# Kernel tuning notes

Hardware: AMD Instinct MI355X
Metric: run time of the kernel (lower is better)

## Reference

```python
import jax, jax.numpy as jnp
import numpy as np

SIREN_OMEGA_0 = 30.0
EPS = 1e-4


def setup_inputs() -> dict:
    key = jax.random.key(0)
    ks = jax.random.split(key, 10)
    B, N, M, IN, OUT = 2, 16384, 1024, 256, 256
    x = jax.random.normal(ks[0], (B, N, IN), dtype=jnp.float32)
    query_coords = jax.random.normal(ks[1], (B, N, 3), dtype=jnp.float32)
    atomic_coords = jax.random.normal(ks[2], (B, M, 3), dtype=jnp.float32)
    # SIREN init (not is_first): bound = sqrt(6/in)/omega_0
    bound = (6.0 / IN) ** 0.5 / SIREN_OMEGA_0
    W = jax.random.uniform(ks[3], (OUT, IN), jnp.float32, -bound, bound)
    b = jax.random.uniform(ks[4], (OUT,), jnp.float32, -bound, bound)
    # freq_net: Linear(3,16) -> Softplus -> Linear(16,1), default torch init
    b1l = 1.0 / np.sqrt(3.0)
    fw1 = jax.random.uniform(ks[5], (16, 3), jnp.float32, -b1l, b1l)
    fb1 = jax.random.uniform(ks[6], (16,), jnp.float32, -b1l, b1l)
    b2l = 1.0 / np.sqrt(16.0)
    fw2 = jax.random.uniform(ks[7], (1, 16), jnp.float32, -b2l, b2l)
    fb2 = jax.random.uniform(ks[8], (1,), jnp.float32, -b2l, b2l)
    return {"x": x, "query_coords": query_coords, "atomic_coords": atomic_coords,
            "W": W, "b": b, "fw1": fw1, "fb1": fb1, "fw2": fw2, "fb2": fb2}


def reference(x, query_coords, atomic_coords, W, b, fw1, fb1, fw2, fb2):
    omega_base = SIREN_OMEGA_0
    # pre_activation = x @ W^T + b : [B, N, OUT]
    pre = jnp.einsum('bni,oi->bno', x, W) + b
    # freq_net(query_coords): Linear -> softplus -> Linear, clamp [0,5], nan->0
    h = jax.nn.softplus(jnp.einsum('bnd,hd->bnh', query_coords, fw1) + fb1)
    local_scale = jnp.einsum('bnh,oh->bno', h, fw2) + fb2  # [B, N, 1]
    local_scale = jnp.nan_to_num(jnp.clip(local_scale, 0.0, 5.0), nan=0.0)
    # pairwise distance [B, N, M] via broadcasted diff, then min over atoms
    diff = query_coords[:, :, None, :] - atomic_coords[:, None, :, :]  # [B,N,M,3]
    dist = jnp.sqrt(jnp.maximum(jnp.sum(diff * diff, axis=-1), EPS))
    min_dist = jnp.min(dist, axis=-1, keepdims=True)  # [B, N, 1]
    omega = omega_base * (1.0 + local_scale * jnp.exp(-min_dist))
    return jnp.sin(omega * pre)
```

## Files before the change

### kernel.cpp

```cpp
#include <hip/hip_runtime.h>
#include <hip/hip_bf16.h>

#define NPTS    32768
#define K_DIM   256
#define O_DIM   256
#define M_ATOMS 1024

typedef __attribute__((ext_vector_type(8))) short short8;
typedef __attribute__((ext_vector_type(4))) float f32x4;

__device__ __forceinline__ unsigned short bf16_rn(float f) {
  unsigned u = __float_as_uint(f);
  unsigned r = u + 0x7FFFu + ((u >> 16) & 1u);
  return (unsigned short)(r >> 16);
}

__device__ __forceinline__ void cvt8(const f32x4 f0, const f32x4 f1,
                                     short8* h, short8* l) {
#pragma unroll
  for (int j = 0; j < 4; ++j) {
    unsigned short h0 = bf16_rn(f0[j]);
    (*h)[j] = (short)h0;
    (*l)[j] = (short)bf16_rn(f0[j] - __uint_as_float((unsigned)h0 << 16));
    unsigned short h1 = bf16_rn(f1[j]);
    (*h)[j + 4] = (short)h1;
    (*l)[j + 4] = (short)bf16_rn(f1[j] - __uint_as_float((unsigned)h1 << 16));
  }
}

__device__ __forceinline__ void async16(void* l, const void* g) {
  __builtin_amdgcn_global_load_lds(
      (const __attribute__((address_space(1))) void*)g,
      (__attribute__((address_space(3))) void*)l, 16, 0, 0);
}

__global__ __launch_bounds__(256) void wprep_kernel(const float* __restrict__ W,
                                                    unsigned short* __restrict__ whF,
                                                    unsigned short* __restrict__ wlF) {
  int t = blockIdx.x * 256 + threadIdx.x;
  int lane = t & 63;
  int ct = (t >> 6) & 15;
  int kc = t >> 10;
  int col = ct * 16 + (lane & 15);
  int k0 = kc * 32 + (lane >> 4) * 8;
  const float* src = W + (size_t)col * K_DIM + k0;
  f32x4 f0 = *(const f32x4*)(src);
  f32x4 f1 = *(const f32x4*)(src + 4);
  short8 h, l;
  cvt8(f0, f1, &h, &l);
  *(short8*)(whF + (size_t)t * 8) = h;
  *(short8*)(wlF + (size_t)t * 8) = l;
}

__global__ __launch_bounds__(256, 2) void fused_kernel(
    const float* __restrict__ x, const float* __restrict__ qc,
    const float* __restrict__ atoms,
    const unsigned short* __restrict__ whF, const unsigned short* __restrict__ wlF,
    const float* __restrict__ bias,
    const float* __restrict__ fw1, const float* __restrict__ fb1,
    const float* __restrict__ fw2, const float* __restrict__ fb2,
    float* __restrict__ out) {
  __shared__ f32x4 bsh[2][2048];
  char* ldsC = (char*)&bsh[0][0];
  const int lane = threadIdx.x & 63;
  const int wave = threadIdx.x >> 6;
  const int lrow = lane & 15;
  const int lk = lane >> 4;
  const int pbase = blockIdx.x * 64 + wave * 16;
  const int row = pbase + lrow;

  float bias_r[16];
#pragma unroll
  for (int ct = 0; ct < 16; ++ct) bias_r[ct] = bias[ct * 16 + lrow];

  const char* whB = (const char*)whF;
  const char* wlB = (const char*)wlF;
  const int toff = wave * 1024 + lane * 16;

  {
    char* db = ldsC;
    const char* gh = whB + toff;
    const char* gl = wlB + toff;
#pragma unroll
    for (int j = 0; j < 4; ++j) {
      async16(db + j * 4096 + wave * 1024, gh + j * 4096);
      async16(db + 16384 + j * 4096 + wave * 1024, gl + j * 4096);
    }
  }

  const float* xr = x + (size_t)row * K_DIM + lk * 8;
  f32x4 a0 = *(const f32x4*)(xr);
  f32x4 a1 = *(const f32x4*)(xr + 4);
  short8 ahi, alo;
  cvt8(a0, a1, &ahi, &alo);

  f32x4 acc[16];
#pragma unroll
  for (int ct = 0; ct < 16; ++ct) acc[ct] = (f32x4){0.f, 0.f, 0.f, 0.f};

  __syncthreads();

  int cur = 0;
  f32x4 a0n, a1n;
#pragma unroll 1
  for (int it = 0; it < 8; ++it) {
    if (it < 7) {
      char* db = ldsC + (cur ^ 1) * 32768;
      const char* gh = whB + (it + 1) * 16384 + toff;
      const char* gl = wlB + (it + 1) * 16384 + toff;
#pragma unroll
      for (int j = 0; j < 4; ++j) {
        async16(db + j * 4096 + wave * 1024, gh + j * 4096);
        async16(db + 16384 + j * 4096 + wave * 1024, gl + j * 4096);
      }
      const float* xn = x + (size_t)row * K_DIM + (it + 1) * 32 + lk * 8;
      a0n = *(const f32x4*)(xn);
      a1n = *(const f32x4*)(xn + 4);
    }
    const char* bp = ldsC + cur * 32768;
#pragma unroll
    for (int ct = 0; ct < 16; ++ct) {
      short8 bh = *(const short8*)(bp + ct * 1024 + lane * 16);
      short8 bl = *(const short8*)(bp + 16384 + ct * 1024 + lane * 16);
      acc[ct] = __builtin_amdgcn_mfma_f32_16x16x32_bf16(ahi, bh, acc[ct], 0, 0, 0);
      acc[ct] = __builtin_amdgcn_mfma_f32_16x16x32_bf16(alo, bh, acc[ct], 0, 0, 0);
      acc[ct] = __builtin_amdgcn_mfma_f32_16x16x32_bf16(ahi, bl, acc[ct], 0, 0, 0);
    }
    __syncthreads();
    if (it < 7) {
      cvt8(a0n, a1n, &ahi, &alo);
      cur ^= 1;
    }
  }

  const int batch = pbase >> 14;
  const float* A = atoms + (size_t)batch * M_ATOMS * 3;
  f32x4* at4 = (f32x4*)ldsC;
  for (int i = threadIdx.x; i < M_ATOMS; i += 256) {
    const float* ap = A + i * 3;
    float ax = ap[0], ay = ap[1], az = ap[2];
    f32x4 v = {ax, ay, az, ax * ax + ay * ay + az * az};
    at4[i] = v;
  }
  __syncthreads();

  const int pt = pbase + lrow;
  const float qx = qc[(size_t)pt * 3 + 0];
  const float qy = qc[(size_t)pt * 3 + 1];
  const float qz = qc[(size_t)pt * 3 + 2];
  float m0 = 3.0e38f, m1 = 3.0e38f, m2 = 3.0e38f, m3 = 3.0e38f;
  const int i0 = lk * 256;
  for (int i = i0; i < i0 + 256; i += 4) {
    f32x4 v0 = at4[i + 0], v1 = at4[i + 1], v2 = at4[i + 2], v3 = at4[i + 3];
    float d;
    d = v0[0] * qx; d = __fmaf_rn(v0[1], qy, d); d = __fmaf_rn(v0[2], qz, d);
    m0 = fminf(m0, __fmaf_rn(d, -2.0f, v0[3]));
    d = v1[0] * qx; d = __fmaf_rn(v1[1], qy, d); d = __fmaf_rn(v1[2], qz, d);
    m1 = fminf(m1, __fmaf_rn(d, -2.0f, v1[3]));
    d = v2[0] * qx; d = __fmaf_rn(v2[1], qy, d); d = __fmaf_rn(v2[2], qz, d);
    m2 = fminf(m2, __fmaf_rn(d, -2.0f, v2[3]));
    d = v3[0] * qx; d = __fmaf_rn(v3[1], qy, d); d = __fmaf_rn(v3[2], qz, d);
    m3 = fminf(m3, __fmaf_rn(d, -2.0f, v3[3]));
  }
  float md = fminf(fminf(m0, m1), fminf(m2, m3));
  md = fminf(md, __shfl_xor(md, 16));
  md = fminf(md, __shfl_xor(md, 32));
  md += qx * qx + qy * qy + qz * qz;
  float mind = sqrtf(fmaxf(md, 1.0e-4f));

  float facc = fb2[0];
#pragma unroll
  for (int j = 0; j < 16; ++j) {
    float z = fw1[j * 3 + 0] * qx + fw1[j * 3 + 1] * qy + fw1[j * 3 + 2] * qz + fb1[j];
    facc += fw2[j] * log1pf(__expf(z));
  }
  float ls = fminf(fmaxf(facc, 0.0f), 5.0f);
  float omega_l = 30.0f * (1.0f + ls * __expf(-mind));

  float om[4];
#pragma unroll
  for (int j = 0; j < 4; ++j) om[j] = __shfl(omega_l, lk * 4 + j);

#pragma unroll
  for (int ct = 0; ct < 16; ++ct) {
#pragma unroll
    for (int j = 0; j < 4; ++j) {
      float pre = acc[ct][j] + bias_r[ct];
      out[(size_t)(pbase + lk * 4 + j) * O_DIM + ct * 16 + lrow] = __sinf(om[j] * pre);
    }
  }
}

extern "C" void kernel_launch(void* const* d_in, const int* in_sizes, int n_in,
                              void* d_out, int out_size, void* d_ws, size_t ws_size,
                              hipStream_t stream) {
  (void)in_sizes; (void)n_in; (void)out_size; (void)ws_size;
  const float* x     = (const float*)d_in[0];
  const float* qc    = (const float*)d_in[1];
  const float* atoms = (const float*)d_in[2];
  const float* W     = (const float*)d_in[3];
  const float* b     = (const float*)d_in[4];
  const float* fw1   = (const float*)d_in[5];
  const float* fb1   = (const float*)d_in[6];
  const float* fw2   = (const float*)d_in[7];
  const float* fb2   = (const float*)d_in[8];
  float* out = (float*)d_out;

  unsigned short* whF = (unsigned short*)d_ws;
  unsigned short* wlF = whF + 65536;

  wprep_kernel<<<32, 256, 0, stream>>>(W, whF, wlF);
  fused_kernel<<<512, 256, 0, stream>>>(x, qc, atoms, whF, wlF, b,
                                        fw1, fb1, fw2, fb2, out);
}
```

Before: 119.5 us.

## Split waves into 2x2 point/column tiles to halve B-fragment LDS reads

Each wave now computes 32 points by 128 output columns instead of 16 points by 256 columns. Every B fragment read from LDS is reused across two A row-tiles, which halves LDS read traffic per MFMA. The x loads per wave double and the min-distance search is split across the wave pair, whose partial minima are now combined through LDS with an extra barrier. The MFMA count and accumulator register count stay the same.

```diff
diff --git a/kernel.cpp b/kernel.cpp
--- a/kernel.cpp
+++ b/kernel.cpp
@@ -64,14 +64,15 @@
   char* ldsC = (char*)&bsh[0][0];
   const int lane = threadIdx.x & 63;
   const int wave = threadIdx.x >> 6;
+  const int ptile = wave >> 1;
+  const int ch = wave & 1;
   const int lrow = lane & 15;
   const int lk = lane >> 4;
-  const int pbase = blockIdx.x * 64 + wave * 16;
-  const int row = pbase + lrow;
-
-  float bias_r[16];
-#pragma unroll
-  for (int ct = 0; ct < 16; ++ct) bias_r[ct] = bias[ct * 16 + lrow];
+  const int pbase = blockIdx.x * 64 + ptile * 32;
+
+  float bias_r[8];
+#pragma unroll
+  for (int ct = 0; ct < 8; ++ct) bias_r[ct] = bias[(ch * 8 + ct) * 16 + lrow];
 
   const char* whB = (const char*)whF;
   const char* wlB = (const char*)wlF;
@@ -88,20 +89,22 @@
     }
   }
 
-  const float* xr = x + (size_t)row * K_DIM + lk * 8;
-  f32x4 a0 = *(const f32x4*)(xr);
-  f32x4 a1 = *(const f32x4*)(xr + 4);
-  short8 ahi, alo;
-  cvt8(a0, a1, &ahi, &alo);
+  const float* xr0 = x + (size_t)(pbase + lrow) * K_DIM + lk * 8;
+  const float* xr1 = x + (size_t)(pbase + 16 + lrow) * K_DIM + lk * 8;
+  f32x4 a00 = *(const f32x4*)(xr0), a01 = *(const f32x4*)(xr0 + 4);
+  f32x4 a10 = *(const f32x4*)(xr1), a11 = *(const f32x4*)(xr1 + 4);
+  short8 ahi0, alo0, ahi1, alo1;
+  cvt8(a00, a01, &ahi0, &alo0);
+  cvt8(a10, a11, &ahi1, &alo1);
 
   f32x4 acc[16];
 #pragma unroll
-  for (int ct = 0; ct < 16; ++ct) acc[ct] = (f32x4){0.f, 0.f, 0.f, 0.f};
+  for (int i = 0; i < 16; ++i) acc[i] = (f32x4){0.f, 0.f, 0.f, 0.f};
 
   __syncthreads();
 
   int cur = 0;
-  f32x4 a0n, a1n;
+  f32x4 n00, n01, n10, n11;
 #pragma unroll 1
   for (int it = 0; it < 8; ++it) {
     if (it < 7) {
@@ -113,22 +116,27 @@
         async16(db + j * 4096 + wave * 1024, gh + j * 4096);
         async16(db + 16384 + j * 4096 + wave * 1024, gl + j * 4096);
       }
-      const float* xn = x + (size_t)row * K_DIM + (it + 1) * 32 + lk * 8;
-      a0n = *(const f32x4*)(xn);
-      a1n = *(const f32x4*)(xn + 4);
-    }
-    const char* bp = ldsC + cur * 32768;
-#pragma unroll
-    for (int ct = 0; ct < 16; ++ct) {
+      const float* p0 = xr0 + (it + 1) * 32;
+      const float* p1 = xr1 + (it + 1) * 32;
+      n00 = *(const f32x4*)(p0); n01 = *(const f32x4*)(p0 + 4);
+      n10 = *(const f32x4*)(p1); n11 = *(const f32x4*)(p1 + 4);
+    }
+    const char* bp = ldsC + cur * 32768 + ch * 8192;
+#pragma unroll
+    for (int ct = 0; ct < 8; ++ct) {
       short8 bh = *(const short8*)(bp + ct * 1024 + lane * 16);
       short8 bl = *(const short8*)(bp + 16384 + ct * 1024 + lane * 16);
-      acc[ct] = __builtin_amdgcn_mfma_f32_16x16x32_bf16(ahi, bh, acc[ct], 0, 0, 0);
-      acc[ct] = __builtin_amdgcn_mfma_f32_16x16x32_bf16(alo, bh, acc[ct], 0, 0, 0);
-      acc[ct] = __builtin_amdgcn_mfma_f32_16x16x32_bf16(ahi, bl, acc[ct], 0, 0, 0);
+      acc[ct]     = __builtin_amdgcn_mfma_f32_16x16x32_bf16(ahi0, bh, acc[ct],     0, 0, 0);
+      acc[8 + ct] = __builtin_amdgcn_mfma_f32_16x16x32_bf16(ahi1, bh, acc[8 + ct], 0, 0, 0);
+      acc[ct]     = __builtin_amdgcn_mfma_f32_16x16x32_bf16(alo0, bh, acc[ct],     0, 0, 0);
+      acc[8 + ct] = __builtin_amdgcn_mfma_f32_16x16x32_bf16(alo1, bh, acc[8 + ct], 0, 0, 0);
+      acc[ct]     = __builtin_amdgcn_mfma_f32_16x16x32_bf16(ahi0, bl, acc[ct],     0, 0, 0);
+      acc[8 + ct] = __builtin_amdgcn_mfma_f32_16x16x32_bf16(ahi1, bl, acc[8 + ct], 0, 0, 0);
     }
     __syncthreads();
     if (it < 7) {
-      cvt8(a0n, a1n, &ahi, &alo);
+      cvt8(n00, n01, &ahi0, &alo0);
+      cvt8(n10, n11, &ahi1, &alo1);
       cur ^= 1;
     }
   }
@@ -136,6 +144,7 @@
   const int batch = pbase >> 14;
   const float* A = atoms + (size_t)batch * M_ATOMS * 3;
   f32x4* at4 = (f32x4*)ldsC;
+  float* red = (float*)(ldsC + 16384);
   for (int i = threadIdx.x; i < M_ATOMS; i += 256) {
     const float* ap = A + i * 3;
     float ax = ap[0], ay = ap[1], az = ap[2];
@@ -144,12 +153,13 @@
   }
   __syncthreads();
 
-  const int pt = pbase + lrow;
+  const int p = lane & 31;
+  const int pt = pbase + p;
   const float qx = qc[(size_t)pt * 3 + 0];
   const float qy = qc[(size_t)pt * 3 + 1];
   const float qz = qc[(size_t)pt * 3 + 2];
   float m0 = 3.0e38f, m1 = 3.0e38f, m2 = 3.0e38f, m3 = 3.0e38f;
-  const int i0 = lk * 256;
+  const int i0 = (ch * 2 + (lane >> 5)) * 256;
   for (int i = i0; i < i0 + 256; i += 4) {
     f32x4 v0 = at4[i + 0], v1 = at4[i + 1], v2 = at4[i + 2], v3 = at4[i + 3];
     float d;
@@ -163,8 +173,13 @@
     m3 = fminf(m3, __fmaf_rn(d, -2.0f, v3[3]));
   }
   float md = fminf(fminf(m0, m1), fminf(m2, m3));
-  md = fminf(md, __shfl_xor(md, 16));
-  md = fminf(md, __shfl_xor(md, 32));
+  red[wave * 64 + lane] = md;
+  __syncthreads();
+  {
+    const int rb = ptile * 128;
+    md = fminf(fminf(red[rb + p], red[rb + 32 + p]),
+               fminf(red[rb + 64 + p], red[rb + 96 + p]));
+  }
   md += qx * qx + qy * qy + qz * qz;
   float mind = sqrtf(fmaxf(md, 1.0e-4f));
 
@@ -177,16 +192,23 @@
   float ls = fminf(fmaxf(facc, 0.0f), 5.0f);
   float omega_l = 30.0f * (1.0f + ls * __expf(-mind));
 
-  float om[4];
-#pragma unroll
-  for (int j = 0; j < 4; ++j) om[j] = __shfl(omega_l, lk * 4 + j);
-
-#pragma unroll
-  for (int ct = 0; ct < 16; ++ct) {
-#pragma unroll
-    for (int j = 0; j < 4; ++j) {
-      float pre = acc[ct][j] + bias_r[ct];
-      out[(size_t)(pbase + lk * 4 + j) * O_DIM + ct * 16 + lrow] = __sinf(om[j] * pre);
+  float om[2][4];
+#pragma unroll
+  for (int t = 0; t < 2; ++t)
+#pragma unroll
+    for (int j = 0; j < 4; ++j)
+      om[t][j] = __shfl(omega_l, t * 16 + lk * 4 + j);
+
+#pragma unroll
+  for (int ct = 0; ct < 8; ++ct) {
+#pragma unroll
+    for (int t = 0; t < 2; ++t) {
+#pragma unroll
+      for (int j = 0; j < 4; ++j) {
+        float pre = acc[t * 8 + ct][j] + bias_r[ct];
+        out[(size_t)(pbase + t * 16 + lk * 4 + j) * O_DIM + (ch * 8 + ct) * 16 + lrow] =
+            __sinf(om[t][j] * pre);
+      }
     }
   }
 }
```

Result: no change. 120.7 us (+1.0%).
